# Kernel tuning notes

Hardware: AMD Instinct MI355X
Metric: run time of the kernel (lower is better)

Reference implementation:

```python
import jax, jax.numpy as jnp
import numpy as np

NEG = jnp.float32(-1e10)

def setup_inputs() -> dict:
    key = jax.random.key(0)
    k1, k2, k3, k4 = jax.random.split(key, 4)
    B, Ns, Nr, D = 64, 512, 256, 1024
    return {
        "span_embeddings": jax.random.normal(k1, (B, Ns, D), dtype=jnp.float32),
        "image_embeddings": jax.random.normal(k2, (B, Nr, D), dtype=jnp.float32),
        "span_mask": jax.random.randint(k3, (B, Ns), 0, 2).astype(jnp.int32),
        "image_mask": jax.random.randint(k4, (B, Nr), 0, 2).astype(jnp.int32),
    }

def reference(span_embeddings, image_embeddings, span_mask, image_mask):
    # pair mask: (B, Ns, Nr) = image_mask[b, None, r] * span_mask[b, s, None]
    mask = (image_mask[:, None, :] * span_mask[:, :, None]).astype(span_embeddings.dtype)
    # QK^T with multiplicative mask, then custom zero->-1e10 masking
    att = jnp.einsum('bsd,brd->bsr', span_embeddings, image_embeddings) * mask
    att = jnp.where(att != 0, att, NEG)
    # spans attend over ROIs
    w_first = jax.nn.softmax(att, axis=-1) * mask
    att_first = jnp.einsum('bsr,brd->bsd', w_first, image_embeddings)
    score = jnp.mean(jnp.square(span_embeddings - att_first))
    # ROIs attend over spans (score_type='both')
    att_t = jnp.swapaxes(att, 1, 2)            # (B, Nr, Ns)
    w_second = jax.nn.softmax(att_t, axis=-1) * jnp.swapaxes(mask, 1, 2)
    att_second = jnp.einsum('brs,bsd->brd', w_second, span_embeddings)
    score = score + jnp.mean(jnp.square(image_embeddings - att_second))
    return score, att_first, att
```

## Files before the change

### kernel.cpp

```cpp
#include <hip/hip_runtime.h>
#include <hip/hip_bf16.h>
#include <math.h>

#define B_  64
#define NS  512
#define NR  256
#define DD  1024
#define NEGV (-1e10f)

typedef __attribute__((ext_vector_type(4))) float f32x4;
typedef __attribute__((ext_vector_type(8))) short bf16x8;

__device__ __forceinline__ unsigned short f2bf(float x) {
    unsigned u = __builtin_bit_cast(unsigned, x);
    unsigned r = u + 0x7FFFu + ((u >> 16) & 1u);
    return (unsigned short)(r >> 16);
}
__device__ __forceinline__ float bf2f(unsigned short h) {
    unsigned u = ((unsigned)h) << 16;
    return __builtin_bit_cast(float, u);
}
__device__ __forceinline__ unsigned pk2(float x, float y) {
    unsigned r;
    asm("v_cvt_pk_bf16_f32 %0, %1, %2" : "=v"(r) : "v"(x), "v"(y));
    return r;
}
__device__ __forceinline__ void pk_hilo(float x, float y, unsigned& h, unsigned& l) {
    h = pk2(x, y);
    const float hx = __builtin_bit_cast(float, h << 16);
    const float hy = __builtin_bit_cast(float, h & 0xFFFF0000u);
    l = pk2(x - hx, y - hy);
}
__device__ __forceinline__ void gload16(const void* g, void* l) {
    __builtin_amdgcn_global_load_lds((const __attribute__((address_space(1))) void*)g,
                                     (__attribute__((address_space(3))) void*)l, 16, 0, 0);
}

__global__ __launch_bounds__(64) void zero_ws(double* ws) {
    if (threadIdx.x == 0) { ws[0] = 0.0; ws[1] = 0.0; }
}

__global__ __launch_bounds__(256) void att_mfma(
    const float* __restrict__ span, const float* __restrict__ image,
    const int* __restrict__ smask, const int* __restrict__ imask,
    float* __restrict__ att, float* __restrict__ rowP, float* __restrict__ colP,
    int doStats) {
    const int b  = blockIdx.z;
    const int s0 = blockIdx.y * 128;
    const int r0 = blockIdx.x * 128;
    __shared__ unsigned short Ah[128][40], Al[128][40], Bh[128][40], Bl[128][40];
    const int tid  = threadIdx.x;
    const int lane = tid & 63;
    const int w    = tid >> 6;
    const int wso  = (w >> 1) * 64;
    const int wro  = (w & 1) * 64;
    const float* Sp = span  + ((size_t)b * NS + s0) * DD;
    const float* Im = image + ((size_t)b * NR + r0) * DD;

    f32x4 acc[4][4];
    #pragma unroll
    for (int i = 0; i < 4; ++i)
        #pragma unroll
        for (int j = 0; j < 4; ++j) acc[i][j] = (f32x4){0.f, 0.f, 0.f, 0.f};

    const int krel = (tid & 7) * 4;
    const int row0 = tid >> 3;
    const int fr   = lane & 15;
    const int fk   = (lane >> 4) * 8;

    for (int k0 = 0; k0 < DD; k0 += 32) {
        #pragma unroll
        for (int p = 0; p < 4; ++p) {
            const int row = row0 + p * 32;
            const float4 a = *reinterpret_cast<const float4*>(Sp + (size_t)row * DD + k0 + krel);
            const float4 c = *reinterpret_cast<const float4*>(Im + (size_t)row * DD + k0 + krel);
            unsigned h0, l0, h1, l1;
            uint2 u;
            pk_hilo(a.x, a.y, h0, l0); pk_hilo(a.z, a.w, h1, l1);
            u.x = h0; u.y = h1; *reinterpret_cast<uint2*>(&Ah[row][krel]) = u;
            u.x = l0; u.y = l1; *reinterpret_cast<uint2*>(&Al[row][krel]) = u;
            pk_hilo(c.x, c.y, h0, l0); pk_hilo(c.z, c.w, h1, l1);
            u.x = h0; u.y = h1; *reinterpret_cast<uint2*>(&Bh[row][krel]) = u;
            u.x = l0; u.y = l1; *reinterpret_cast<uint2*>(&Bl[row][krel]) = u;
        }
        __syncthreads();
        bf16x8 ah[4], al[4], bh[4], bl[4];
        #pragma unroll
        for (int mf = 0; mf < 4; ++mf) {
            ah[mf] = *reinterpret_cast<const bf16x8*>(&Ah[wso + mf * 16 + fr][fk]);
            al[mf] = *reinterpret_cast<const bf16x8*>(&Al[wso + mf * 16 + fr][fk]);
            bh[mf] = *reinterpret_cast<const bf16x8*>(&Bh[wro + mf * 16 + fr][fk]);
            bl[mf] = *reinterpret_cast<const bf16x8*>(&Bl[wro + mf * 16 + fr][fk]);
        }
        #pragma unroll
        for (int mf = 0; mf < 4; ++mf)
            #pragma unroll
            for (int nf = 0; nf < 4; ++nf) {
                acc[mf][nf] = __builtin_amdgcn_mfma_f32_16x16x32_bf16(ah[mf], bh[nf], acc[mf][nf], 0, 0, 0);
                acc[mf][nf] = __builtin_amdgcn_mfma_f32_16x16x32_bf16(ah[mf], bl[nf], acc[mf][nf], 0, 0, 0);
                acc[mf][nf] = __builtin_amdgcn_mfma_f32_16x16x32_bf16(al[mf], bh[nf], acc[mf][nf], 0, 0, 0);
            }
        __syncthreads();
    }

    float* rowLDS = reinterpret_cast<float*>(&Ah[0][0]);
    float* colLDS = rowLDS + 256;
    const int fq = lane >> 4;
    int imv[4];
    #pragma unroll
    for (int nf = 0; nf < 4; ++nf) imv[nf] = imask[b * NR + r0 + wro + nf * 16 + fr];
    float cmax[4] = {-3.4e38f, -3.4e38f, -3.4e38f, -3.4e38f};
    #pragma unroll
    for (int mf = 0; mf < 4; ++mf) {
        #pragma unroll
        for (int i = 0; i < 4; ++i) {
            const int s = s0 + wso + mf * 16 + fq * 4 + i;
            const int sm = smask[b * NS + s];
            float* orow = att + ((size_t)b * NS + s) * NR + r0 + wro;
            float vj[4];
            #pragma unroll
            for (int nf = 0; nf < 4; ++nf) {
                float v = acc[mf][nf][i] * (float)(sm * imv[nf]);
                v = (v != 0.0f) ? v : NEGV;
                orow[nf * 16 + fr] = v;
                vj[nf] = v;
                cmax[nf] = fmaxf(cmax[nf], v);
            }
            if (doStats) {
                float rm = fmaxf(fmaxf(vj[0], vj[1]), fmaxf(vj[2], vj[3]));
                rm = fmaxf(rm, __shfl_xor(rm, 1));
                rm = fmaxf(rm, __shfl_xor(rm, 2));
                rm = fmaxf(rm, __shfl_xor(rm, 4));
                rm = fmaxf(rm, __shfl_xor(rm, 8));
                if (fr == 0) rowLDS[(wso + mf * 16 + fq * 4 + i) * 2 + (w & 1)] = rm;
            }
        }
    }
    if (doStats) {
        #pragma unroll
        for (int nf = 0; nf < 4; ++nf) {
            cmax[nf] = fmaxf(cmax[nf], __shfl_xor(cmax[nf], 16));
            cmax[nf] = fmaxf(cmax[nf], __shfl_xor(cmax[nf], 32));
        }
        if (lane < 16) {
            #pragma unroll
            for (int nf = 0; nf < 4; ++nf)
                colLDS[(wro + nf * 16 + lane) * 2 + (w >> 1)] = cmax[nf];
        }
        __syncthreads();
        if (tid < 128) {
            rowP[((size_t)b * NS + s0 + tid) * 2 + blockIdx.x] =
                fmaxf(rowLDS[tid * 2 + 0], rowLDS[tid * 2 + 1]);
        } else {
            const int c = tid - 128;
            colP[((size_t)b * NR + r0 + c) * 4 + blockIdx.y] =
                fmaxf(colLDS[c * 2 + 0], colLDS[c * 2 + 1]);
        }
    }
}

__global__ __launch_bounds__(256) void combine_max(
    const float* __restrict__ rowP, const float* __restrict__ colP,
    float* __restrict__ m1, float* __restrict__ m2,
    float* __restrict__ rowsum1, float* __restrict__ colsum2) {
    const int idx = blockIdx.x * 256 + threadIdx.x;
    if (idx < B_ * NS) {
        m1[idx] = fmaxf(rowP[(size_t)idx * 2 + 0], rowP[(size_t)idx * 2 + 1]);
        rowsum1[idx] = 0.0f;
    } else if (idx < B_ * NS + B_ * NR) {
        const int j = idx - B_ * NS;
        m2[j] = fmaxf(fmaxf(colP[(size_t)j * 4 + 0], colP[(size_t)j * 4 + 1]),
                      fmaxf(colP[(size_t)j * 4 + 2], colP[(size_t)j * 4 + 3]));
        colsum2[j] = 0.0f;
    }
}

__global__ __launch_bounds__(256) void transpose_swz(
    const float* __restrict__ src, unsigned short* __restrict__ dst, int N) {
    const int b = blockIdx.z, n0 = blockIdx.y * 32, d0 = blockIdx.x * 32;
    __shared__ unsigned short T[32][36];
    const int t = threadIdx.x;
    {
        const int n = t >> 3, dq = (t & 7) * 4;
        const float4 v = *reinterpret_cast<const float4*>(src + ((size_t)b * N + n0 + n) * DD + d0 + dq);
        T[dq + 0][n] = f2bf(v.x); T[dq + 1][n] = f2bf(v.y);
        T[dq + 2][n] = f2bf(v.z); T[dq + 3][n] = f2bf(v.w);
    }
    __syncthreads();
    {
        const int d = t >> 3, nq = (t & 7) * 4;
        const int dg = d0 + d;
        const int base = n0 + nq;
        const int pos = (base & 63) ^ ((dg & 7) << 3);
        const size_t idx = ((size_t)b * DD + dg) * N + (base & ~63) + pos;
        *reinterpret_cast<ushort4*>(dst + idx) = *reinterpret_cast<const ushort4*>(&T[d][nq]);
    }
}

__global__ __launch_bounds__(256) void build_w12(
    const float* __restrict__ att, const int* __restrict__ smask,
    const int* __restrict__ imask,
    const float* __restrict__ m1, const float* __restrict__ m2,
    unsigned short* __restrict__ w1g, unsigned short* __restrict__ w2g,
    float* __restrict__ rowsum1, float* __restrict__ colsum2) {
    const int b = blockIdx.z, s0 = blockIdx.y * 64, r0 = blockIdx.x * 64;
    __shared__ unsigned short T[64][68];
    __shared__ float m2s[64], ims[64], sms[64];
    const int tid = threadIdx.x;
    if (tid < 64) {
        m2s[tid] = m2[b * NR + r0 + tid];
        ims[tid] = (float)imask[b * NR + r0 + tid];
        sms[tid] = (float)smask[b * NS + s0 + tid];
    }
    __syncthreads();
    {
        const int srow = tid >> 2, rg = (tid & 3) * 16;
        const int s = s0 + srow;
        const float m1v = m1[b * NS + s];
        const float* arow = att + ((size_t)b * NS + s) * NR + r0;
        const int w1swz = (s & 7) << 3;
        unsigned short* w1row = w1g + ((size_t)b * NS + s) * NR + r0;
        float rsum = 0.0f;
        #pragma unroll
        for (int g = 0; g < 4; ++g) {
            const int rr = rg + g * 4;
            const float4 a = *reinterpret_cast<const float4*>(arow + rr);
            const float e0 = __expf(a.x - m1v);
            const float e1 = __expf(a.y - m1v);
            const float e2 = __expf(a.z - m1v);
            const float e3 = __expf(a.w - m1v);
            rsum += (e0 + e1) + (e2 + e3);
            uint2 u;
            u.x = pk2(e0 * ims[rr + 0], e1 * ims[rr + 1]);
            u.y = pk2(e2 * ims[rr + 2], e3 * ims[rr + 3]);
            *reinterpret_cast<uint2*>(w1row + (rr ^ w1swz)) = u;
            const float q0 = __expf(a.x - m2s[rr + 0]);
            const float q1 = __expf(a.y - m2s[rr + 1]);
            const float q2 = __expf(a.z - m2s[rr + 2]);
            const float q3 = __expf(a.w - m2s[rr + 3]);
            const unsigned t0 = pk2(q0, q1), t1 = pk2(q2, q3);
            T[rr + 0][srow] = (unsigned short)(t0 & 0xFFFF);
            T[rr + 1][srow] = (unsigned short)(t0 >> 16);
            T[rr + 2][srow] = (unsigned short)(t1 & 0xFFFF);
            T[rr + 3][srow] = (unsigned short)(t1 >> 16);
        }
        rsum += __shfl_xor(rsum, 1);
        rsum += __shfl_xor(rsum, 2);
        if ((tid & 3) == 0) atomicAdd(&rowsum1[b * NS + s], rsum);
    }
    __syncthreads();
    {
        const int rl = tid >> 2, sg = (tid & 3) * 16;
        const int w2swz = (rl & 7) << 3;
        unsigned short* w2row = w2g + ((size_t)b * NR + r0 + rl) * NS + s0;
        float csum = 0.0f;
        #pragma unroll
        for (int g = 0; g < 4; ++g) {
            const int ss = sg + g * 4;
            const ushort4 t = *reinterpret_cast<const ushort4*>(&T[rl][ss]);
            csum += (bf2f(t.x) + bf2f(t.y)) + (bf2f(t.z) + bf2f(t.w));
            ushort4 o;
            o.x = (sms[ss + 0] != 0.0f) ? t.x : (unsigned short)0;
            o.y = (sms[ss + 1] != 0.0f) ? t.y : (unsigned short)0;
            o.z = (sms[ss + 2] != 0.0f) ? t.z : (unsigned short)0;
            o.w = (sms[ss + 3] != 0.0f) ? t.w : (unsigned short)0;
            *reinterpret_cast<ushort4*>(w2row + (ss ^ w2swz)) = o;
        }
        csum += __shfl_xor(csum, 1);
        csum += __shfl_xor(csum, 2);
        if ((tid & 3) == 0) atomicAdd(&colsum2[b * NR + r0 + rl], csum);
    }
}

template<int KTOT, int MT, bool WOUT, int WIDX>
__global__ __launch_bounds__(256) void gemm_apply(
    const unsigned short* __restrict__ Ag, const unsigned short* __restrict__ Btg,
    const float* __restrict__ ref, float* __restrict__ outp,
    const int* __restrict__ rmask, const float* __restrict__ rsum,
    double* __restrict__ wsum) {
    const int b = blockIdx.z, m0 = blockIdx.y * 64, d0 = blockIdx.x * 256;
    __shared__ unsigned short As[64 * 64];
    __shared__ unsigned short Bs[256 * 64];
    __shared__ float redsum[256];
    const int tid = threadIdx.x, lane = tid & 63, w = tid >> 6;
    const int fr = lane & 15, fq = lane >> 4;
    f32x4 acc[4][4];
    #pragma unroll
    for (int i = 0; i < 4; ++i)
        #pragma unroll
        for (int j = 0; j < 4; ++j) acc[i][j] = (f32x4){0.f, 0.f, 0.f, 0.f};

    const int srow = tid >> 3;
    const int scol = (tid & 7) * 16;
    for (int kc = 0; kc < KTOT / 64; ++kc) {
        const char* asrc = (const char*)(Ag + ((size_t)b * MT + m0) * KTOT) + kc * 128 + scol;
        #pragma unroll
        for (int c = 0; c < 2; ++c)
            gload16(asrc + (size_t)(c * 32 + srow) * (KTOT * 2), (char*)As + (c * 256 + tid) * 16);
        const char* bsrc = (const char*)(Btg + ((size_t)b * DD + d0) * KTOT) + kc * 128 + scol;
        #pragma unroll
        for (int c = 0; c < 8; ++c)
            gload16(bsrc + (size_t)(c * 32 + srow) * (KTOT * 2), (char*)Bs + (c * 256 + tid) * 16);
        __syncthreads();
        #pragma unroll
        for (int ks = 0; ks < 2; ++ks) {
            bf16x8 aF[4], bF[4];
            #pragma unroll
            for (int mf = 0; mf < 4; ++mf) {
                const int row = mf * 16 + fr;
                const int pos = (ks * 32 + fq * 8) ^ ((row & 7) << 3);
                aF[mf] = *reinterpret_cast<const bf16x8*>(&As[row * 64 + pos]);
            }
            #pragma unroll
            for (int nf = 0; nf < 4; ++nf) {
                const int row = w * 64 + nf * 16 + fr;
                const int pos = (ks * 32 + fq * 8) ^ ((row & 7) << 3);
                bF[nf] = *reinterpret_cast<const bf16x8*>(&Bs[row * 64 + pos]);
            }
            #pragma unroll
            for (int mf = 0; mf < 4; ++mf)
                #pragma unroll
                for (int nf = 0; nf < 4; ++nf)
                    acc[mf][nf] = __builtin_amdgcn_mfma_f32_16x16x32_bf16(aF[mf], bF[nf], acc[mf][nf], 0, 0, 0);
        }
        __syncthreads();
    }
    float sumsq = 0.0f;
    #pragma unroll
    for (int mf = 0; mf < 4; ++mf) {
        #pragma unroll
        for (int i = 0; i < 4; ++i) {
            const int row = m0 + mf * 16 + fq * 4 + i;
            const size_t gidx = (size_t)b * MT + row;
            const float fac = (float)rmask[gidx] / rsum[gidx];
            const size_t base = gidx * DD + d0 + w * 64;
            #pragma unroll
            for (int nf = 0; nf < 4; ++nf) {
                const float v = acc[mf][nf][i] * fac;
                const float rv = ref[base + nf * 16 + fr];
                if constexpr (WOUT) outp[base + nf * 16 + fr] = v;
                const float dx = rv - v;
                sumsq += dx * dx;
            }
        }
    }
    redsum[tid] = sumsq; __syncthreads();
    for (int off = 128; off; off >>= 1) {
        if (tid < off) redsum[tid] += redsum[tid + off];
        __syncthreads();
    }
    if (tid == 0) atomicAdd(wsum + WIDX, (double)redsum[0]);
}

__global__ __launch_bounds__(256) void first_kernel(
    const float* __restrict__ span, const float* __restrict__ image,
    const int* __restrict__ smask, const int* __restrict__ imask,
    const float* __restrict__ att, float* __restrict__ att_first,
    double* __restrict__ ws) {
    const int b  = blockIdx.y;
    const int s0 = blockIdx.x * 32;
    __shared__ float wT[256][36];
    __shared__ float Is[32][132];
    __shared__ float red[256];
    const int tid  = threadIdx.x;
    const int lane = tid & 63, wave = tid >> 6;
    for (int i = 0; i < 8; ++i) {
        const int srel = wave * 8 + i;
        const int s    = s0 + srel;
        const float4 v = *reinterpret_cast<const float4*>(att + ((size_t)b * NS + s) * NR + lane * 4);
        float m = fmaxf(fmaxf(v.x, v.y), fmaxf(v.z, v.w));
        #pragma unroll
        for (int off = 32; off; off >>= 1) m = fmaxf(m, __shfl_xor(m, off));
        float4 e;
        e.x = expf(v.x - m); e.y = expf(v.y - m); e.z = expf(v.z - m); e.w = expf(v.w - m);
        float sum = e.x + e.y + e.z + e.w;
        #pragma unroll
        for (int off = 32; off; off >>= 1) sum += __shfl_xor(sum, off);
        const float fac = (float)smask[b * NS + s] / sum;
        const int4 im4 = *reinterpret_cast<const int4*>(imask + b * NR + lane * 4);
        wT[lane * 4 + 0][srel] = e.x * fac * (float)im4.x;
        wT[lane * 4 + 1][srel] = e.y * fac * (float)im4.y;
        wT[lane * 4 + 2][srel] = e.z * fac * (float)im4.z;
        wT[lane * 4 + 3][srel] = e.w * fac * (float)im4.w;
    }
    __syncthreads();
    float sumsq = 0.0f;
    const int txd = tid & 31;
    const int tys = tid >> 5;
    const float* Ib = image + (size_t)b * NR * DD;
    for (int dc = 0; dc < 8; ++dc) {
        const int d0 = dc * 128;
        float acc[4][4] = {};
        for (int rc = 0; rc < 8; ++rc) {
            const int r0 = rc * 32;
            {
                const int rr = tid >> 3;
                const int cb = tid & 7;
                const float* src = Ib + (size_t)(r0 + rr) * DD + d0;
                #pragma unroll
                for (int q = 0; q < 4; ++q)
                    *reinterpret_cast<float4*>(&Is[rr][(cb + 8 * q) * 4]) =
                        *reinterpret_cast<const float4*>(src + (cb + 8 * q) * 4);
            }
            __syncthreads();
            #pragma unroll 4
            for (int rr = 0; rr < 32; ++rr) {
                const float4 wv = *reinterpret_cast<const float4*>(&wT[r0 + rr][tys * 4]);
                const float4 iv = *reinterpret_cast<const float4*>(&Is[rr][txd * 4]);
                const float wvv[4] = {wv.x, wv.y, wv.z, wv.w};
                const float ivv[4] = {iv.x, iv.y, iv.z, iv.w};
                #pragma unroll
                for (int i = 0; i < 4; ++i)
                    #pragma unroll
                    for (int j = 0; j < 4; ++j)
                        acc[i][j] += wvv[i] * ivv[j];
            }
            __syncthreads();
        }
        #pragma unroll
        for (int i = 0; i < 4; ++i) {
            const int s = s0 + tys * 4 + i;
            const size_t base = ((size_t)b * NS + s) * DD + d0 + txd * 4;
            const float4 af = {acc[i][0], acc[i][1], acc[i][2], acc[i][3]};
            *reinterpret_cast<float4*>(att_first + base) = af;
            const float4 sp = *reinterpret_cast<const float4*>(span + base);
            float dx;
            dx = sp.x - af.x; sumsq += dx * dx;
            dx = sp.y - af.y; sumsq += dx * dx;
            dx = sp.z - af.z; sumsq += dx * dx;
            dx = sp.w - af.w; sumsq += dx * dx;
        }
    }
    red[tid] = sumsq; __syncthreads();
    for (int off = 128; off; off >>= 1) {
        if (tid < off) red[tid] += red[tid + off];
        __syncthreads();
    }
    if (tid == 0) atomicAdd(ws, (double)red[0]);
}

__global__ __launch_bounds__(256) void second_kernel(
    const float* __restrict__ span, const float* __restrict__ image,
    const int* __restrict__ smask, const int* __restrict__ imask,
    const float* __restrict__ att, double* __restrict__ ws) {
    const int b  = blockIdx.y;
    const int r0 = blockIdx.x * 32;
    __shared__ float w2s[32][36];
    __shared__ float Ss[32][132];
    __shared__ float mArr[32], fArr[32];
    __shared__ float redm[8][32];
    __shared__ float red[256];
    const int tid = threadIdx.x;
    const int rr = tid & 31, q = tid >> 5;
    const float* attb = att + (size_t)b * NS * NR + r0 + rr;
    float mloc = -3.4e38f;
    for (int t = 0; t < 64; ++t)
        mloc = fmaxf(mloc, attb[(size_t)(q * 64 + t) * NR]);
    redm[q][rr] = mloc;
    __syncthreads();
    if (tid < 32) {
        float m = redm[0][tid];
        #pragma unroll
        for (int qq = 1; qq < 8; ++qq) m = fmaxf(m, redm[qq][tid]);
        mArr[tid] = m;
    }
    __syncthreads();
    const float mcol = mArr[rr];
    float sloc = 0.0f;
    for (int t = 0; t < 64; ++t)
        sloc += expf(attb[(size_t)(q * 64 + t) * NR] - mcol);
    redm[q][rr] = sloc;
    __syncthreads();
    if (tid < 32) {
        float s = 0.0f;
        #pragma unroll
        for (int qq = 0; qq < 8; ++qq) s += redm[qq][tid];
        fArr[tid] = (float)imask[b * NR + r0 + tid] / s;
    }
    __syncthreads();
    float sumsq = 0.0f;
    const int txd = tid & 31;
    const int tyr = tid >> 5;
    const float* Sb = span + (size_t)b * NS * DD;
    for (int dc = 0; dc < 8; ++dc) {
        const int d0 = dc * 128;
        float acc[4][4] = {};
        for (int sc = 0; sc < 16; ++sc) {
            const int sb0 = sc * 32;
            {
                const int sr = tid >> 3;
                const int cb = tid & 7;
                const float* src = Sb + (size_t)(sb0 + sr) * DD + d0;
                #pragma unroll
                for (int qq = 0; qq < 4; ++qq)
                    *reinterpret_cast<float4*>(&Ss[sr][(cb + 8 * qq) * 4]) =
                        *reinterpret_cast<const float4*>(src + (cb + 8 * qq) * 4);
            }
            {
                const int ss = tid >> 3;
                const int rq = (tid & 7) * 4;
                const int s  = sb0 + ss;
                const float4 v = *reinterpret_cast<const float4*>(att + ((size_t)b * NS + s) * NR + r0 + rq);
                const float smv = (float)smask[b * NS + s];
                float4 wv;
                wv.x = expf(v.x - mArr[rq + 0]) * fArr[rq + 0] * smv;
                wv.y = expf(v.y - mArr[rq + 1]) * fArr[rq + 1] * smv;
                wv.z = expf(v.z - mArr[rq + 2]) * fArr[rq + 2] * smv;
                wv.w = expf(v.w - mArr[rq + 3]) * fArr[rq + 3] * smv;
                *reinterpret_cast<float4*>(&w2s[ss][rq]) = wv;
            }
            __syncthreads();
            #pragma unroll 4
            for (int ss = 0; ss < 32; ++ss) {
                const float4 wv = *reinterpret_cast<const float4*>(&w2s[ss][tyr * 4]);
                const float4 sv = *reinterpret_cast<const float4*>(&Ss[ss][txd * 4]);
                const float wvv[4] = {wv.x, wv.y, wv.z, wv.w};
                const float svv[4] = {sv.x, sv.y, sv.z, sv.w};
                #pragma unroll
                for (int i = 0; i < 4; ++i)
                    #pragma unroll
                    for (int j = 0; j < 4; ++j)
                        acc[i][j] += wvv[i] * svv[j];
            }
            __syncthreads();
        }
        #pragma unroll
        for (int i = 0; i < 4; ++i) {
            const int r = r0 + tyr * 4 + i;
            const float4 iv = *reinterpret_cast<const float4*>(image + ((size_t)b * NR + r) * DD + d0 + txd * 4);
            float dx;
            dx = iv.x - acc[i][0]; sumsq += dx * dx;
            dx = iv.y - acc[i][1]; sumsq += dx * dx;
            dx = iv.z - acc[i][2]; sumsq += dx * dx;
            dx = iv.w - acc[i][3]; sumsq += dx * dx;
        }
    }
    red[tid] = sumsq; __syncthreads();
    for (int off = 128; off; off >>= 1) {
        if (tid < off) red[tid] += red[tid + off];
        __syncthreads();
    }
    if (tid == 0) atomicAdd(ws + 1, (double)red[0]);
}

__global__ __launch_bounds__(64) void score_kernel(const double* __restrict__ ws, float* __restrict__ out) {
    if (threadIdx.x == 0) {
        out[0] = (float)(ws[0] / (double)((size_t)B_ * NS * DD) +
                         ws[1] / (double)((size_t)B_ * NR * DD));
    }
}

extern "C" void kernel_launch(void* const* d_in, const int* in_sizes, int n_in,
                              void* d_out, int out_size, void* d_ws, size_t ws_size,
                              hipStream_t stream) {
    const float* span  = (const float*)d_in[0];
    const float* image = (const float*)d_in[1];
    const int*   smask = (const int*)d_in[2];
    const int*   imask = (const int*)d_in[3];
    float* out       = (float*)d_out;
    float* att_first = out + 1;
    float* att       = out + 1 + (size_t)B_ * NS * DD;

    char* base = (char*)d_ws;
    double* wsum = (double*)base;
    float* m1      = (float*)(base + 512);
    float* m2      = m1 + (size_t)B_ * NS;
    float* rowsum1 = m2 + (size_t)B_ * NR;
    float* colsum2 = rowsum1 + (size_t)B_ * NS;
    float* rowP    = colsum2 + (size_t)B_ * NR;
    float* colP    = rowP + (size_t)B_ * NS * 2;
    char* X0 = (char*)(colP + (size_t)B_ * NR * 4);
    unsigned short* imgT = (unsigned short*)X0;
    unsigned short* w1g  = (unsigned short*)(X0 + (size_t)B_ * DD * NR * 2);
    unsigned short* spT  = (unsigned short*)X0;
    unsigned short* w2g  = (unsigned short*)(X0 + (size_t)B_ * DD * NS * 2);
    const size_t NEED = (size_t)(X0 - base) + (size_t)B_ * DD * NS * 2 + (size_t)B_ * NS * NR * 2;
    const int wsok = (ws_size >= NEED) ? 1 : 0;

    zero_ws<<<dim3(1), dim3(64), 0, stream>>>(wsum);
    att_mfma<<<dim3(NR / 128, NS / 128, B_), dim3(256), 0, stream>>>(
        span, image, smask, imask, att, rowP, colP, wsok);

    if (wsok) {
        combine_max<<<dim3((B_ * NS + B_ * NR) / 256), dim3(256), 0, stream>>>(
            rowP, colP, m1, m2, rowsum1, colsum2);
        transpose_swz<<<dim3(DD / 32, NR / 32, B_), dim3(256), 0, stream>>>(image, imgT, NR);
        build_w12<<<dim3(NR / 64, NS / 64, B_), dim3(256), 0, stream>>>(
            att, smask, imask, m1, m2, w1g, w2g, rowsum1, colsum2);
        gemm_apply<NR, NS, true, 0><<<dim3(DD / 256, NS / 64, B_), dim3(256), 0, stream>>>(
            w1g, imgT, span, att_first, smask, rowsum1, wsum);
        transpose_swz<<<dim3(DD / 32, NS / 32, B_), dim3(256), 0, stream>>>(span, spT, NS);
        gemm_apply<NS, NR, false, 1><<<dim3(DD / 256, NR / 64, B_), dim3(256), 0, stream>>>(
            w2g, spT, image, nullptr, imask, colsum2, wsum);
    } else {
        first_kernel<<<dim3(NS / 32, B_), dim3(256), 0, stream>>>(span, image, smask, imask, att, att_first, wsum);
        second_kernel<<<dim3(NR / 32, B_), dim3(256), 0, stream>>>(span, image, smask, imask, att, wsum);
    }
    score_kernel<<<dim3(1), dim3(64), 0, stream>>>(wsum, out);
}
```

Measured before the change: 310.5 us.

## Fuse softmax weight construction into the two apply GEMMs, dropping build_w12

Removes the separate build_w12 pass that wrote bf16 softmax weight matrices and row/column sums to global memory. Each GEMM now reads fp32 att tiles directly, computes the exponentials, masks and converts to bf16 into LDS, and reduces the row or column sums inside the block. This saves a kernel launch, the global writes and reads of both weight matrices, and the atomics. In exchange, att is re-read by every d-tile block (four times per GEMM), the exp work is repeated per d-tile, and gemm2 performs scalar swizzled LDS stores.

Result: no change. 311.6 us (+0.3%).

```diff
diff --git a/kernel.cpp b/kernel.cpp
--- a/kernel.cpp
+++ b/kernel.cpp
@@ -15,10 +15,6 @@
     unsigned u = __builtin_bit_cast(unsigned, x);
     unsigned r = u + 0x7FFFu + ((u >> 16) & 1u);
     return (unsigned short)(r >> 16);
-}
-__device__ __forceinline__ float bf2f(unsigned short h) {
-    unsigned u = ((unsigned)h) << 16;
-    return __builtin_bit_cast(float, u);
 }
 __device__ __forceinline__ unsigned pk2(float x, float y) {
     unsigned r;
@@ -161,17 +157,14 @@
 
 __global__ __launch_bounds__(256) void combine_max(
     const float* __restrict__ rowP, const float* __restrict__ colP,
-    float* __restrict__ m1, float* __restrict__ m2,
-    float* __restrict__ rowsum1, float* __restrict__ colsum2) {
+    float* __restrict__ m1, float* __restrict__ m2) {
     const int idx = blockIdx.x * 256 + threadIdx.x;
     if (idx < B_ * NS) {
         m1[idx] = fmaxf(rowP[(size_t)idx * 2 + 0], rowP[(size_t)idx * 2 + 1]);
-        rowsum1[idx] = 0.0f;
     } else if (idx < B_ * NS + B_ * NR) {
         const int j = idx - B_ * NS;
         m2[j] = fmaxf(fmaxf(colP[(size_t)j * 4 + 0], colP[(size_t)j * 4 + 1]),
                       fmaxf(colP[(size_t)j * 4 + 2], colP[(size_t)j * 4 + 3]));
-        colsum2[j] = 0.0f;
     }
 }
 
@@ -197,110 +190,75 @@
     }
 }
 
-__global__ __launch_bounds__(256) void build_w12(
-    const float* __restrict__ att, const int* __restrict__ smask,
-    const int* __restrict__ imask,
-    const float* __restrict__ m1, const float* __restrict__ m2,
-    unsigned short* __restrict__ w1g, unsigned short* __restrict__ w2g,
-    float* __restrict__ rowsum1, float* __restrict__ colsum2) {
-    const int b = blockIdx.z, s0 = blockIdx.y * 64, r0 = blockIdx.x * 64;
-    __shared__ unsigned short T[64][68];
-    __shared__ float m2s[64], ims[64], sms[64];
-    const int tid = threadIdx.x;
-    if (tid < 64) {
-        m2s[tid] = m2[b * NR + r0 + tid];
-        ims[tid] = (float)imask[b * NR + r0 + tid];
-        sms[tid] = (float)smask[b * NS + s0 + tid];
-    }
-    __syncthreads();
-    {
-        const int srow = tid >> 2, rg = (tid & 3) * 16;
-        const int s = s0 + srow;
-        const float m1v = m1[b * NS + s];
-        const float* arow = att + ((size_t)b * NS + s) * NR + r0;
-        const int w1swz = (s & 7) << 3;
-        unsigned short* w1row = w1g + ((size_t)b * NS + s) * NR + r0;
-        float rsum = 0.0f;
-        #pragma unroll
-        for (int g = 0; g < 4; ++g) {
-            const int rr = rg + g * 4;
-            const float4 a = *reinterpret_cast<const float4*>(arow + rr);
-            const float e0 = __expf(a.x - m1v);
-            const float e1 = __expf(a.y - m1v);
-            const float e2 = __expf(a.z - m1v);
-            const float e3 = __expf(a.w - m1v);
-            rsum += (e0 + e1) + (e2 + e3);
-            uint2 u;
-            u.x = pk2(e0 * ims[rr + 0], e1 * ims[rr + 1]);
-            u.y = pk2(e2 * ims[rr + 2], e3 * ims[rr + 3]);
-            *reinterpret_cast<uint2*>(w1row + (rr ^ w1swz)) = u;
-            const float q0 = __expf(a.x - m2s[rr + 0]);
-            const float q1 = __expf(a.y - m2s[rr + 1]);
-            const float q2 = __expf(a.z - m2s[rr + 2]);
-            const float q3 = __expf(a.w - m2s[rr + 3]);
-            const unsigned t0 = pk2(q0, q1), t1 = pk2(q2, q3);
-            T[rr + 0][srow] = (unsigned short)(t0 & 0xFFFF);
-            T[rr + 1][srow] = (unsigned short)(t0 >> 16);
-            T[rr + 2][srow] = (unsigned short)(t1 & 0xFFFF);
-            T[rr + 3][srow] = (unsigned short)(t1 >> 16);
-        }
-        rsum += __shfl_xor(rsum, 1);
-        rsum += __shfl_xor(rsum, 2);
-        if ((tid & 3) == 0) atomicAdd(&rowsum1[b * NS + s], rsum);
-    }
-    __syncthreads();
-    {
-        const int rl = tid >> 2, sg = (tid & 3) * 16;
-        const int w2swz = (rl & 7) << 3;
-        unsigned short* w2row = w2g + ((size_t)b * NR + r0 + rl) * NS + s0;
-        float csum = 0.0f;
-        #pragma unroll
-        for (int g = 0; g < 4; ++g) {
-            const int ss = sg + g * 4;
-            const ushort4 t = *reinterpret_cast<const ushort4*>(&T[rl][ss]);
-            csum += (bf2f(t.x) + bf2f(t.y)) + (bf2f(t.z) + bf2f(t.w));
-            ushort4 o;
-            o.x = (sms[ss + 0] != 0.0f) ? t.x : (unsigned short)0;
-            o.y = (sms[ss + 1] != 0.0f) ? t.y : (unsigned short)0;
-            o.z = (sms[ss + 2] != 0.0f) ? t.z : (unsigned short)0;
-            o.w = (sms[ss + 3] != 0.0f) ? t.w : (unsigned short)0;
-            *reinterpret_cast<ushort4*>(w2row + (ss ^ w2swz)) = o;
-        }
-        csum += __shfl_xor(csum, 1);
-        csum += __shfl_xor(csum, 2);
-        if ((tid & 3) == 0) atomicAdd(&colsum2[b * NR + r0 + rl], csum);
-    }
-}
-
-template<int KTOT, int MT, bool WOUT, int WIDX>
-__global__ __launch_bounds__(256) void gemm_apply(
-    const unsigned short* __restrict__ Ag, const unsigned short* __restrict__ Btg,
-    const float* __restrict__ ref, float* __restrict__ outp,
-    const int* __restrict__ rmask, const float* __restrict__ rsum,
-    double* __restrict__ wsum) {
+__global__ __launch_bounds__(256) void gemm1_fused(
+    const float* __restrict__ att, const unsigned short* __restrict__ imgT,
+    const float* __restrict__ span,
+    const int* __restrict__ smask, const int* __restrict__ imask,
+    const float* __restrict__ m1,
+    float* __restrict__ att_first, double* __restrict__ wsum) {
     const int b = blockIdx.z, m0 = blockIdx.y * 64, d0 = blockIdx.x * 256;
     __shared__ unsigned short As[64 * 64];
     __shared__ unsigned short Bs[256 * 64];
     __shared__ float redsum[256];
+    __shared__ float m1s[64], sms[64], rowsumS[64];
+    __shared__ float ims[256];
     const int tid = threadIdx.x, lane = tid & 63, w = tid >> 6;
     const int fr = lane & 15, fq = lane >> 4;
+    if (tid < 64) {
+        m1s[tid] = m1[b * NS + m0 + tid];
+        sms[tid] = (float)smask[b * NS + m0 + tid];
+    }
+    ims[tid] = (float)imask[b * NR + tid];
     f32x4 acc[4][4];
     #pragma unroll
     for (int i = 0; i < 4; ++i)
         #pragma unroll
         for (int j = 0; j < 4; ++j) acc[i][j] = (f32x4){0.f, 0.f, 0.f, 0.f};
 
+    const int arow = tid >> 2;
+    const int acg  = (tid & 3) * 16;
+    const int akey = (arow & 7) << 3;
     const int srow = tid >> 3;
     const int scol = (tid & 7) * 16;
-    for (int kc = 0; kc < KTOT / 64; ++kc) {
-        const char* asrc = (const char*)(Ag + ((size_t)b * MT + m0) * KTOT) + kc * 128 + scol;
-        #pragma unroll
-        for (int c = 0; c < 2; ++c)
-            gload16(asrc + (size_t)(c * 32 + srow) * (KTOT * 2), (char*)As + (c * 256 + tid) * 16);
-        const char* bsrc = (const char*)(Btg + ((size_t)b * DD + d0) * KTOT) + kc * 128 + scol;
+    float rsum = 0.0f;
+    __syncthreads();
+
+    for (int kc = 0; kc < NR / 64; ++kc) {
+        const char* bsrc = (const char*)(imgT + ((size_t)b * DD + d0) * NR) + kc * 128 + scol;
         #pragma unroll
         for (int c = 0; c < 8; ++c)
-            gload16(bsrc + (size_t)(c * 32 + srow) * (KTOT * 2), (char*)Bs + (c * 256 + tid) * 16);
+            gload16(bsrc + (size_t)(c * 32 + srow) * (NR * 2), (char*)Bs + (c * 256 + tid) * 16);
+        {
+            const float* ap = att + ((size_t)b * NS + m0 + arow) * NR + kc * 64 + acg;
+            const float m1v = m1s[arow];
+            const float4 a0 = *reinterpret_cast<const float4*>(ap);
+            const float4 a1 = *reinterpret_cast<const float4*>(ap + 4);
+            const float4 a2 = *reinterpret_cast<const float4*>(ap + 8);
+            const float4 a3 = *reinterpret_cast<const float4*>(ap + 12);
+            float e[16];
+            e[0] = __expf(a0.x - m1v); e[1] = __expf(a0.y - m1v);
+            e[2] = __expf(a0.z - m1v); e[3] = __expf(a0.w - m1v);
+            e[4] = __expf(a1.x - m1v); e[5] = __expf(a1.y - m1v);
+            e[6] = __expf(a1.z - m1v); e[7] = __expf(a1.w - m1v);
+            e[8] = __expf(a2.x - m1v); e[9] = __expf(a2.y - m1v);
+            e[10] = __expf(a2.z - m1v); e[11] = __expf(a2.w - m1v);
+            e[12] = __expf(a3.x - m1v); e[13] = __expf(a3.y - m1v);
+            e[14] = __expf(a3.z - m1v); e[15] = __expf(a3.w - m1v);
+            #pragma unroll
+            for (int j = 0; j < 16; ++j) rsum += e[j];
+            const int ib = kc * 64 + acg;
+            uint4 u;
+            u.x = pk2(e[0] * ims[ib + 0], e[1] * ims[ib + 1]);
+            u.y = pk2(e[2] * ims[ib + 2], e[3] * ims[ib + 3]);
+            u.z = pk2(e[4] * ims[ib + 4], e[5] * ims[ib + 5]);
+            u.w = pk2(e[6] * ims[ib + 6], e[7] * ims[ib + 7]);
+            *reinterpret_cast<uint4*>(&As[arow * 64 + (acg ^ akey)]) = u;
+            u.x = pk2(e[8] * ims[ib + 8], e[9] * ims[ib + 9]);
+            u.y = pk2(e[10] * ims[ib + 10], e[11] * ims[ib + 11]);
+            u.z = pk2(e[12] * ims[ib + 12], e[13] * ims[ib + 13]);
+            u.w = pk2(e[14] * ims[ib + 14], e[15] * ims[ib + 15]);
+            *reinterpret_cast<uint4*>(&As[arow * 64 + ((acg + 8) ^ akey)]) = u;
+        }
         __syncthreads();
         #pragma unroll
         for (int ks = 0; ks < 2; ++ks) {
@@ -325,20 +283,24 @@
         }
         __syncthreads();
     }
+    rsum += __shfl_xor(rsum, 1);
+    rsum += __shfl_xor(rsum, 2);
+    if ((tid & 3) == 0) rowsumS[arow] = rsum;
+    __syncthreads();
+
     float sumsq = 0.0f;
     #pragma unroll
     for (int mf = 0; mf < 4; ++mf) {
         #pragma unroll
         for (int i = 0; i < 4; ++i) {
-            const int row = m0 + mf * 16 + fq * 4 + i;
-            const size_t gidx = (size_t)b * MT + row;
-            const float fac = (float)rmask[gidx] / rsum[gidx];
-            const size_t base = gidx * DD + d0 + w * 64;
+            const int row = mf * 16 + fq * 4 + i;
+            const float fac = sms[row] / rowsumS[row];
+            const size_t base = ((size_t)b * NS + m0 + row) * DD + d0 + w * 64;
             #pragma unroll
             for (int nf = 0; nf < 4; ++nf) {
                 const float v = acc[mf][nf][i] * fac;
-                const float rv = ref[base + nf * 16 + fr];
-                if constexpr (WOUT) outp[base + nf * 16 + fr] = v;
+                const float rv = span[base + nf * 16 + fr];
+                att_first[base + nf * 16 + fr] = v;
                 const float dx = rv - v;
                 sumsq += dx * dx;
             }
@@ -349,7 +311,127 @@
         if (tid < off) redsum[tid] += redsum[tid + off];
         __syncthreads();
     }
-    if (tid == 0) atomicAdd(wsum + WIDX, (double)redsum[0]);
+    if (tid == 0) atomicAdd(wsum, (double)redsum[0]);
+}
+
+__global__ __launch_bounds__(256) void gemm2_fused(
+    const float* __restrict__ att, const unsigned short* __restrict__ spT,
+    const float* __restrict__ image,
+    const int* __restrict__ smask, const int* __restrict__ imask,
+    const float* __restrict__ m2, double* __restrict__ wsum) {
+    const int b = blockIdx.z, r0 = blockIdx.y * 64, d0 = blockIdx.x * 256;
+    __shared__ unsigned short As[64 * 64];
+    __shared__ unsigned short Bs[256 * 64];
+    __shared__ float redsum[256];
+    __shared__ float m2s[64], imsv[64], colsumS[64];
+    __shared__ float smsK[512];
+    __shared__ float cs4[4][64];
+    const int tid = threadIdx.x, lane = tid & 63, w = tid >> 6;
+    const int fr = lane & 15, fq = lane >> 4;
+    if (tid < 64) {
+        m2s[tid] = m2[b * NR + r0 + tid];
+        imsv[tid] = (float)imask[b * NR + r0 + tid];
+    }
+    smsK[tid]       = (float)smask[b * NS + tid];
+    smsK[tid + 256] = (float)smask[b * NS + 256 + tid];
+    f32x4 acc[4][4];
+    #pragma unroll
+    for (int i = 0; i < 4; ++i)
+        #pragma unroll
+        for (int j = 0; j < 4; ++j) acc[i][j] = (f32x4){0.f, 0.f, 0.f, 0.f};
+
+    const int asr = tid >> 2;
+    const int arg = (tid & 3) * 16;
+    const int srow = tid >> 3;
+    const int scol = (tid & 7) * 16;
+    float csum[16];
+    #pragma unroll
+    for (int j = 0; j < 16; ++j) csum[j] = 0.0f;
+    __syncthreads();
+
+    for (int kc = 0; kc < NS / 64; ++kc) {
+        const char* bsrc = (const char*)(spT + ((size_t)b * DD + d0) * NS) + kc * 128 + scol;
+        #pragma unroll
+        for (int c = 0; c < 8; ++c)
+            gload16(bsrc + (size_t)(c * 32 + srow) * (NS * 2), (char*)Bs + (c * 256 + tid) * 16);
+        {
+            const float* ap = att + ((size_t)b * NS + kc * 64 + asr) * NR + r0 + arg;
+            const float smv = smsK[kc * 64 + asr];
+            const float4 a0 = *reinterpret_cast<const float4*>(ap);
+            const float4 a1 = *reinterpret_cast<const float4*>(ap + 4);
+            const float4 a2 = *reinterpret_cast<const float4*>(ap + 8);
+            const float4 a3 = *reinterpret_cast<const float4*>(ap + 12);
+            const float av[16] = {a0.x, a0.y, a0.z, a0.w, a1.x, a1.y, a1.z, a1.w,
+                                  a2.x, a2.y, a2.z, a2.w, a3.x, a3.y, a3.z, a3.w};
+            const int slo = asr & 7;
+            const int shi = asr >> 3;
+            #pragma unroll
+            for (int j = 0; j < 16; ++j) {
+                const int r = arg + j;
+                const float e = __expf(av[j] - m2s[r]);
+                csum[j] += e;
+                const int pos = slo | ((shi ^ (r & 7)) << 3);
+                As[r * 64 + pos] = f2bf(e * smv);
+            }
+        }
+        __syncthreads();
+        #pragma unroll
+        for (int ks = 0; ks < 2; ++ks) {
+            bf16x8 aF[4], bF[4];
+            #pragma unroll
+            for (int mf = 0; mf < 4; ++mf) {
+                const int row = mf * 16 + fr;
+                const int pos = (ks * 32 + fq * 8) ^ ((row & 7) << 3);
+                aF[mf] = *reinterpret_cast<const bf16x8*>(&As[row * 64 + pos]);
+            }
+            #pragma unroll
+            for (int nf = 0; nf < 4; ++nf) {
+                const int row = w * 64 + nf * 16 + fr;
+                const int pos = (ks * 32 + fq * 8) ^ ((row & 7) << 3);
+                bF[nf] = *reinterpret_cast<const bf16x8*>(&Bs[row * 64 + pos]);
+            }
+            #pragma unroll
+            for (int mf = 0; mf < 4; ++mf)
+                #pragma unroll
+                for (int nf = 0; nf < 4; ++nf)
+                    acc[mf][nf] = __builtin_amdgcn_mfma_f32_16x16x32_bf16(aF[mf], bF[nf], acc[mf][nf], 0, 0, 0);
+        }
+        __syncthreads();
+    }
+    #pragma unroll
+    for (int j = 0; j < 16; ++j) {
+        float v = csum[j];
+        v += __shfl_xor(v, 4);
+        v += __shfl_xor(v, 8);
+        v += __shfl_xor(v, 16);
+        v += __shfl_xor(v, 32);
+        if (lane < 4) cs4[w][lane * 16 + j] = v;
+    }
+    __syncthreads();
+    if (tid < 64) colsumS[tid] = (cs4[0][tid] + cs4[1][tid]) + (cs4[2][tid] + cs4[3][tid]);
+    __syncthreads();
+
+    float sumsq = 0.0f;
+    #pragma unroll
+    for (int mf = 0; mf < 4; ++mf) {
+        #pragma unroll
+        for (int i = 0; i < 4; ++i) {
+            const int row = mf * 16 + fq * 4 + i;
+            const float fac = imsv[row] / colsumS[row];
+            const size_t base = ((size_t)b * NR + r0 + row) * DD + d0 + w * 64;
+            #pragma unroll
+            for (int nf = 0; nf < 4; ++nf) {
+                const float dx = image[base + nf * 16 + fr] - acc[mf][nf][i] * fac;
+                sumsq += dx * dx;
+            }
+        }
+    }
+    redsum[tid] = sumsq; __syncthreads();
+    for (int off = 128; off; off >>= 1) {
+        if (tid < off) redsum[tid] += redsum[tid + off];
+        __syncthreads();
+    }
+    if (tid == 0) atomicAdd(wsum + 1, (double)redsum[0]);
 }
 
 __global__ __launch_bounds__(256) void first_kernel(
@@ -563,18 +645,14 @@
 
     char* base = (char*)d_ws;
     double* wsum = (double*)base;
-    float* m1      = (float*)(base + 512);
-    float* m2      = m1 + (size_t)B_ * NS;
-    float* rowsum1 = m2 + (size_t)B_ * NR;
-    float* colsum2 = rowsum1 + (size_t)B_ * NS;
-    float* rowP    = colsum2 + (size_t)B_ * NR;
-    float* colP    = rowP + (size_t)B_ * NS * 2;
+    float* m1   = (float*)(base + 512);
+    float* m2   = m1 + (size_t)B_ * NS;
+    float* rowP = m2 + (size_t)B_ * NR;
+    float* colP = rowP + (size_t)B_ * NS * 2;
     char* X0 = (char*)(colP + (size_t)B_ * NR * 4);
     unsigned short* imgT = (unsigned short*)X0;
-    unsigned short* w1g  = (unsigned short*)(X0 + (size_t)B_ * DD * NR * 2);
     unsigned short* spT  = (unsigned short*)X0;
-    unsigned short* w2g  = (unsigned short*)(X0 + (size_t)B_ * DD * NS * 2);
-    const size_t NEED = (size_t)(X0 - base) + (size_t)B_ * DD * NS * 2 + (size_t)B_ * NS * NR * 2;
+    const size_t NEED = (size_t)(X0 - base) + (size_t)B_ * DD * NS * 2;
     const int wsok = (ws_size >= NEED) ? 1 : 0;
 
     zero_ws<<<dim3(1), dim3(64), 0, stream>>>(wsum);
@@ -583,15 +661,13 @@
 
     if (wsok) {
         combine_max<<<dim3((B_ * NS + B_ * NR) / 256), dim3(256), 0, stream>>>(
-            rowP, colP, m1, m2, rowsum1, colsum2);
+            rowP, colP, m1, m2);
         transpose_swz<<<dim3(DD / 32, NR / 32, B_), dim3(256), 0, stream>>>(image, imgT, NR);
-        build_w12<<<dim3(NR / 64, NS / 64, B_), dim3(256), 0, stream>>>(
-            att, smask, imask, m1, m2, w1g, w2g, rowsum1, colsum2);
-        gemm_apply<NR, NS, true, 0><<<dim3(DD / 256, NS / 64, B_), dim3(256), 0, stream>>>(
-            w1g, imgT, span, att_first, smask, rowsum1, wsum);
+        gemm1_fused<<<dim3(DD / 256, NS / 64, B_), dim3(256), 0, stream>>>(
+            att, imgT, span, smask, imask, m1, att_first, wsum);
         transpose_swz<<<dim3(DD / 32, NS / 32, B_), dim3(256), 0, stream>>>(span, spT, NS);
-        gemm_apply<NS, NR, false, 1><<<dim3(DD / 256, NR / 64, B_), dim3(256), 0, stream>>>(
-            w2g, spT, image, nullptr, imask, colsum2, wsum);
+        gemm2_fused<<<dim3(DD / 256, NR / 64, B_), dim3(256), 0, stream>>>(
+            att, spT, image, smask, imask, m2, wsum);
     } else {
         first_kernel<<<dim3(NS / 32, B_), dim3(256), 0, stream>>>(span, image, smask, imask, att, att_first, wsum);
         second_kernel<<<dim3(NR / 32, B_), dim3(256), 0, stream>>>(span, image, smask, imask, att, wsum);
```
